# Optimization experiments

Measured on AMD Instinct MI355X. Metric: run time of the kernel, lower is better.

## Reference

```python
import jax, jax.numpy as jnp
import numpy as np

HEADS = 4
EPS_LN = 1e-5
EPS_NORM = 1e-12

def conv1x1(x, w):
    # x: [B,C,T,H,W], w: [O,C] (Conv3d kernel_size=1, no bias)
    return jnp.einsum('oc,bcthw->bothw', w, x)

def dwconv3(x, w):
    # depthwise Conv3d 3x3x3, padding=1; w: [C,1,3,3,3]
    return jax.lax.conv_general_dilated(
        x, w, window_strides=(1, 1, 1), padding='SAME',
        dimension_numbers=('NCDHW', 'OIDHW', 'NCDHW'),
        feature_group_count=x.shape[1])

def layernorm_c(x, w, b):
    # LayerNorm over channel dim (torch LN applied after b c t h w -> b (thw) c)
    m = jnp.mean(x, axis=1, keepdims=True)
    v = jnp.mean(jnp.square(x - m), axis=1, keepdims=True)
    xn = (x - m) * jax.lax.rsqrt(v + EPS_LN)
    return xn * w[None, :, None, None, None] + b[None, :, None, None, None]

def l2norm(x):
    n = jnp.sqrt(jnp.sum(jnp.square(x), axis=-1, keepdims=True))
    return x / jnp.maximum(n, EPS_NORM)

def attention_c(x, qkv_w, qkv_dw_w, proj_w, temperature):
    B, C, T, H, W = x.shape
    qkv = dwconv3(conv1x1(x, qkv_w), qkv_dw_w)  # [B,3C,T,H,W]
    q, k, v = jnp.split(qkv, 3, axis=1)
    def to_heads(a):
        return a.reshape(B, HEADS, C // HEADS, T * H * W)  # b head c (thw)
    q, k, v = to_heads(q), to_heads(k), to_heads(v)
    q = l2norm(q)
    k = l2norm(k)
    # channel attention: [b,h,c,c] score matrix scaled by learnable temperature
    attn = jnp.einsum('bhcn,bhdn->bhcd', q, k) * temperature[None]
    attn = jax.nn.softmax(attn, axis=-1)
    out = jnp.einsum('bhcd,bhdn->bhcn', attn, v)
    out = out.reshape(B, C, T, H, W)
    return conv1x1(out, proj_w)

def feedforward(x, pin_w, ffn_dw_w, pout_w):
    h = conv1x1(x, pin_w)            # [B,2H,T,H,W]
    h = dwconv3(h, ffn_dw_w)
    x1, x2 = jnp.split(h, 2, axis=1)
    g = jax.nn.gelu(x1, approximate=False) * x2
    return conv1x1(g, pout_w)

def setup_inputs() -> dict:
    key = jax.random.key(0)
    ks = jax.random.split(key, 8)
    C, T, H, W = 192, 10, 64, 64
    Hf = int(C * 2.66)  # 510
    s = 0.05
    return {
        'x': jax.random.normal(ks[0], (1, C, T, H, W), jnp.float32),
        'ln1_w': jnp.ones((C,), jnp.float32),
        'ln1_b': jnp.zeros((C,), jnp.float32),
        'qkv_w': jax.random.normal(ks[1], (3 * C, C), jnp.float32) * s,
        'qkv_dw_w': jax.random.normal(ks[2], (3 * C, 1, 3, 3, 3), jnp.float32) * s,
        'proj_w': jax.random.normal(ks[3], (C, C), jnp.float32) * s,
        'temperature': jnp.ones((HEADS, 1, 1), jnp.float32),
        'ln2_w': jnp.ones((C,), jnp.float32),
        'ln2_b': jnp.zeros((C,), jnp.float32),
        'pin_w': jax.random.normal(ks[4], (2 * Hf, C), jnp.float32) * s,
        'ffn_dw_w': jax.random.normal(ks[5], (2 * Hf, 1, 3, 3, 3), jnp.float32) * s,
        'pout_w': jax.random.normal(ks[6], (C, Hf), jnp.float32) * s,
    }

def reference(x, ln1_w, ln1_b, qkv_w, qkv_dw_w, proj_w, temperature,
              ln2_w, ln2_b, pin_w, ffn_dw_w, pout_w):
    y = x + attention_c(layernorm_c(x, ln1_w, ln1_b), qkv_w, qkv_dw_w, proj_w, temperature)
    out = y + feedforward(layernorm_c(y, ln2_w, ln2_b), pin_w, ffn_dw_w, pout_w)
    return out
```

## Files before the change

kernel.cpp:

```cpp
#include <hip/hip_runtime.h>
#include <math.h>

#define NPOS 40960
#define TT 10
#define HH 64
#define WW 64
#define HWP 4096
#define CIN 192
#define C3 576
#define NHEADS 4
#define CHD 48
#define HF 510
#define GNB 80
#define GCHUNK 512

typedef unsigned short u16;
typedef unsigned int   u32;
typedef __bf16 bf16x8 __attribute__((ext_vector_type(8)));
typedef __bf16 bf16x2 __attribute__((ext_vector_type(2)));
typedef float  f32x4  __attribute__((ext_vector_type(4)));
typedef u16    u16x8  __attribute__((ext_vector_type(8)));
typedef u32    u32x4  __attribute__((ext_vector_type(4)));

__device__ __forceinline__ float b2f(u16 u) {
    return __uint_as_float(((unsigned int)u) << 16);
}
__device__ __forceinline__ u16 f2b(float f) {
    unsigned int i = __float_as_uint(f);
    unsigned int r = (i + 0x7FFFu + ((i >> 16) & 1u)) >> 16;
    return (u16)r;
}
__device__ __forceinline__ float gelu_exact(float v) {
    return 0.5f * v * (1.0f + erff(v * 0.70710678118654752f));
}

__device__ __forceinline__ float dot2bf(u32 a, u32 b, float c) {
#if __has_builtin(__builtin_amdgcn_fdot2_f32_bf16)
    return __builtin_amdgcn_fdot2_f32_bf16(
        __builtin_bit_cast(bf16x2, a), __builtin_bit_cast(bf16x2, b), c, false);
#else
    float a0 = b2f((u16)(a & 0xffffu)), a1 = b2f((u16)(a >> 16));
    float b0 = b2f((u16)(b & 0xffffu)), b1 = b2f((u16)(b >> 16));
    return fmaf(a1, b1, fmaf(a0, b0, c));
#endif
}
__device__ __forceinline__ u32 alignp(u32 hi, u32 lo) {
#if __has_builtin(__builtin_amdgcn_alignbit)
    return __builtin_amdgcn_alignbit(hi, lo, 16);
#else
    return (lo >> 16) | (hi << 16);
#endif
}

#define GLD_LDS16(g, l) __builtin_amdgcn_global_load_lds( \
    (const __attribute__((address_space(1))) void*)(g), \
    (__attribute__((address_space(3))) void*)(l), 16, 0, 0)

__global__ void cvt_pad_k(const float* __restrict__ src, u16* __restrict__ dst,
                          int rs, int cs, int rd, int cd) {
    int idx = blockIdx.x * 256 + threadIdx.x;
    if (idx >= rd * cd) return;
    int r = idx / cd, c = idx % cd;
    float v = (r < rs && c < cs) ? src[r * cs + c] : 0.f;
    dst[idx] = f2b(v);
}

template<typename InT>
__global__ __launch_bounds__(256) void lnt_k(const InT* __restrict__ X,
                                             const float* __restrict__ w,
                                             const float* __restrict__ b,
                                             u16* __restrict__ Xt) {
    __shared__ float sm[CIN][65];
    __shared__ float ps[4][64], ps2[4][64];
    __shared__ float smean[64], srstd[64];
    __shared__ float sw[CIN], sb[CIN];
    const int tid = threadIdx.x;
    const int n0 = blockIdx.x * 64;
    if (tid < CIN) { sw[tid] = w[tid]; sb[tid] = b[tid]; }
    if constexpr (sizeof(InT) == 4) {
        #pragma unroll
        for (int i = 0; i < 12; ++i) {
            int e = i * 256 + tid;
            int c = e >> 4, p4 = (e & 15) * 4;
            float4 v = *(const float4*)((const float*)X + (size_t)c * NPOS + n0 + p4);
            sm[c][p4 + 0] = v.x; sm[c][p4 + 1] = v.y;
            sm[c][p4 + 2] = v.z; sm[c][p4 + 3] = v.w;
        }
    } else {
        #pragma unroll
        for (int i = 0; i < 6; ++i) {
            int e = i * 256 + tid;
            int c = e >> 3, p8 = (e & 7) * 8;
            u16x8 v = *(const u16x8*)((const u16*)X + (size_t)c * NPOS + n0 + p8);
            #pragma unroll
            for (int j = 0; j < 8; ++j) sm[c][p8 + j] = b2f(v[j]);
        }
    }
    __syncthreads();
    int g = tid >> 6, nn = tid & 63;
    float s = 0.f, s2 = 0.f;
    for (int c = g * 48; c < g * 48 + 48; ++c) {
        float v = sm[c][nn];
        s += v; s2 += v * v;
    }
    ps[g][nn] = s; ps2[g][nn] = s2;
    __syncthreads();
    if (g == 0) {
        float t = ps[0][nn] + ps[1][nn] + ps[2][nn] + ps[3][nn];
        float t2 = ps2[0][nn] + ps2[1][nn] + ps2[2][nn] + ps2[3][nn];
        float m = t / CIN;
        float var = t2 / CIN - m * m;
        smean[nn] = m;
        srstd[nn] = rsqrtf(var + 1e-5f);
    }
    __syncthreads();
    #pragma unroll
    for (int i = 0; i < 6; ++i) {
        int e = i * 256 + tid;
        int nl = e / 24, cg = e % 24;
        int c0 = cg * 8;
        float m = smean[nl], rs_ = srstd[nl];
        u16x8 o;
        #pragma unroll
        for (int j = 0; j < 8; ++j) {
            float v = (sm[c0 + j][nl] - m) * rs_ * sw[c0 + j] + sb[c0 + j];
            o[j] = f2b(v);
        }
        *(u16x8*)(Xt + (size_t)(n0 + nl) * CIN + c0) = o;
    }
}

__global__ __launch_bounds__(256) void transpose_k(const u16* __restrict__ src,
                                                   u16* __restrict__ dst, int C) {
    __shared__ float sm[64][65];
    const int tid = threadIdx.x;
    const int n0 = blockIdx.x * 64;
    const int cb = blockIdx.y * 64;
    #pragma unroll
    for (int i = 0; i < 2; ++i) {
        int e = i * 256 + tid;
        int cl = e >> 3, nn8 = (e & 7) * 8;
        u16x8 v = *(const u16x8*)(src + (size_t)(cb + cl) * NPOS + n0 + nn8);
        #pragma unroll
        for (int j = 0; j < 8; ++j) sm[cl][nn8 + j] = b2f(v[j]);
    }
    __syncthreads();
    #pragma unroll
    for (int i = 0; i < 2; ++i) {
        int e = i * 256 + tid;
        int nl = e >> 3, c0 = (e & 7) * 8;
        u16x8 o;
        #pragma unroll
        for (int j = 0; j < 8; ++j) o[j] = f2b(sm[c0 + j][nl]);
        *(u16x8*)(dst + (size_t)(n0 + nl) * C + cb + c0) = o;
    }
}

__global__ __launch_bounds__(256) void glu_t_k(const u16* __restrict__ hconv,
                                               u16* __restrict__ gt) {
    __shared__ float sm[64][65];
    const int tid = threadIdx.x;
    const int n0 = blockIdx.x * 64;
    const int cb = blockIdx.y * 64;
    #pragma unroll
    for (int i = 0; i < 2; ++i) {
        int e = i * 256 + tid;
        int cl = e >> 3, nn8 = (e & 7) * 8;
        int c = cb + cl;
        if (c < HF) {
            u16x8 va = *(const u16x8*)(hconv + (size_t)c * NPOS + n0 + nn8);
            u16x8 vb = *(const u16x8*)(hconv + (size_t)(c + HF) * NPOS + n0 + nn8);
            #pragma unroll
            for (int j = 0; j < 8; ++j)
                sm[cl][nn8 + j] = gelu_exact(b2f(va[j])) * b2f(vb[j]);
        } else {
            #pragma unroll
            for (int j = 0; j < 8; ++j) sm[cl][nn8 + j] = 0.f;
        }
    }
    __syncthreads();
    #pragma unroll
    for (int i = 0; i < 2; ++i) {
        int e = i * 256 + tid;
        int nl = e >> 3, c0 = (e & 7) * 8;
        u16x8 o;
        #pragma unroll
        for (int j = 0; j < 8; ++j) o[j] = f2b(sm[c0 + j][nl]);
        *(u16x8*)(gt + (size_t)(n0 + nl) * 512 + cb + c0) = o;
    }
}

template<int KP, typename OutT, typename ResT, bool RESID>
__global__ __launch_bounds__(256) void gemm_mfma_k(
    const u16* __restrict__ A, const u16* __restrict__ Bt, int O,
    const ResT* __restrict__ resid, OutT* __restrict__ outp)
{
    constexpr int NT = KP / 32;
    __shared__ u16 As[2][128 * 32];
    __shared__ u16 Bs[2][128 * 32];
    const int tid  = threadIdx.x;
    const int lane = tid & 63;
    const int wv   = tid >> 6;
    const int lo = lane & 15, hi = lane >> 4;
    const int m_blk = blockIdx.y * 128;
    const int n_blk = blockIdx.x * 128;

    int bb0 = (0 * 4 + wv) * 1024 + lane * 16;
    int bb1 = (1 * 4 + wv) * 1024 + lane * 16;
    const int r0 = bb0 >> 6, c80 = (bb0 >> 4) & 3;
    const int r1 = bb1 >> 6, c81 = (bb1 >> 4) & 3;

    auto stage = [&](int buf, int k0) {
        GLD_LDS16(A  + (size_t)(m_blk + r0) * KP + k0 + c80 * 8, (char*)&As[buf][0] + (0 * 4 + wv) * 1024);
        GLD_LDS16(A  + (size_t)(m_blk + r1) * KP + k0 + c81 * 8, (char*)&As[buf][0] + (1 * 4 + wv) * 1024);
        GLD_LDS16(Bt + (size_t)(n_blk + r0) * KP + k0 + c80 * 8, (char*)&Bs[buf][0] + (0 * 4 + wv) * 1024);
        GLD_LDS16(Bt + (size_t)(n_blk + r1) * KP + k0 + c81 * 8, (char*)&Bs[buf][0] + (1 * 4 + wv) * 1024);
    };

    f32x4 acc[4][4];
    const f32x4 zero = {0.f, 0.f, 0.f, 0.f};
    #pragma unroll
    for (int mt = 0; mt < 4; ++mt)
        #pragma unroll
        for (int nt = 0; nt < 4; ++nt) acc[mt][nt] = zero;

    stage(0, 0);
    __syncthreads();

    #pragma unroll
    for (int t = 0; t < NT; ++t) {
        if (t + 1 < NT) stage((t + 1) & 1, (t + 1) * 32);
        const u16* Ab = &As[t & 1][0] + (wv & 1) * 64 * 32;
        const u16* Bb = &Bs[t & 1][0] + (wv >> 1) * 64 * 32;
        bf16x8 a[4], b[4];
        #pragma unroll
        for (int q = 0; q < 4; ++q) {
            a[q] = *(const bf16x8*)(Ab + (q * 16 + lo) * 32 + hi * 8);
            b[q] = *(const bf16x8*)(Bb + (q * 16 + lo) * 32 + hi * 8);
        }
        #pragma unroll
        for (int mt = 0; mt < 4; ++mt)
            #pragma unroll
            for (int nt = 0; nt < 4; ++nt)
                acc[mt][nt] = __builtin_amdgcn_mfma_f32_16x16x32_bf16(
                    a[mt], b[nt], acc[mt][nt], 0, 0, 0);
        __syncthreads();
    }

    const int m_base = m_blk + (wv & 1) * 64;
    const int n_base = n_blk + (wv >> 1) * 64;
    #pragma unroll
    for (int mt = 0; mt < 4; ++mt) {
        #pragma unroll
        for (int r = 0; r < 4; ++r) {
            int m = m_base + mt * 16 + hi * 4 + r;
            if (m < O) {
                size_t rowoff = (size_t)m * NPOS;
                #pragma unroll
                for (int nt = 0; nt < 4; ++nt) {
                    int n = n_base + nt * 16 + lo;
                    float v = acc[mt][nt][r];
                    if (RESID) {
                        if constexpr (sizeof(ResT) == 2) v += b2f(((const u16*)resid)[rowoff + n]);
                        else                             v += ((const float*)resid)[rowoff + n];
                    }
                    if constexpr (sizeof(OutT) == 2) outp[rowoff + n] = (OutT)f2b(v);
                    else                             outp[rowoff + n] = (OutT)v;
                }
            }
        }
    }
}

__global__ __launch_bounds__(256) void dwconv_k(const u16* __restrict__ in,
                                                u16* __restrict__ outp,
                                                const float* __restrict__ wgt)
{
    const int lane = threadIdx.x & 63;
    const int wv   = threadIdx.x >> 6;
    const int c    = blockIdx.x >> 1;
    const int hb   = blockIdx.x & 1;
    const int h    = hb * 32 + wv * 8 + (lane >> 3);
    const int w0c  = (lane & 7) * 8;
    const bool wl0 = (lane & 7) == 0;
    const bool wl7 = (lane & 7) == 7;
    const bool hup = (h > 0), hdn = (h < HH - 1);
    u32 W01[9], W2h[9];
    {
        const float* wc = wgt + c * 27;
        #pragma unroll
        for (int i = 0; i < 9; ++i) {
            float a = wc[i * 3 + 0], b = wc[i * 3 + 1], d = wc[i * 3 + 2];
            W01[i] = (u32)f2b(a) | ((u32)f2b(b) << 16);
            W2h[i] = ((u32)f2b(d)) << 16;
        }
    }
    const u16* base = in   + (size_t)c * (TT * HWP);
    u16*       ob   = outp + (size_t)c * (TT * HWP);

    u32x4 zv = {0u, 0u, 0u, 0u};
    u32x4 ld[2][3];
    auto issue = [&](int ph, int ts) {
        const u16* rp = base + (size_t)ts * HWP + h * WW + w0c;
        ld[ph][0] = hup ? *(const u32x4*)(rp - WW) : zv;
        ld[ph][1] = *(const u32x4*)(rp);
        ld[ph][2] = hdn ? *(const u32x4*)(rp + WW) : zv;
    };

    float acc[3][8];
    #pragma unroll
    for (int o_ = 0; o_ < 3; ++o_)
        #pragma unroll
        for (int j = 0; j < 8; ++j) acc[o_][j] = 0.f;

    issue(0, 0);
    #pragma unroll
    for (int ts = 0; ts < TT; ++ts) {
        const int cb = ts & 1, nb = cb ^ 1;
        if (ts + 1 < TT) issue(nb, ts + 1);
        #pragma unroll
        for (int dh = 0; dh < 3; ++dh) {
            u32 P0 = ld[cb][dh][0], P1 = ld[cb][dh][1];
            u32 P2 = ld[cb][dh][2], P3 = ld[cb][dh][3];
            u32 Pm = __shfl(P3, lane - 1); Pm = wl0 ? 0u : Pm;
            u32 Pp = __shfl(P0, lane + 1); Pp = wl7 ? 0u : Pp;
            u32 S0 = alignp(P0, Pm), S1 = alignp(P1, P0);
            u32 S2 = alignp(P2, P1), S3 = alignp(P3, P2);
            u32 S4 = alignp(Pp, P3);
            #pragma unroll
            for (int tp = 0; tp < 3; ++tp) {
                int o_;
                if (tp == 2) { if (ts < 1) continue; o_ = (ts - 1) % 3; }
                else if (tp == 1) { o_ = ts % 3; }
                else { if (ts + 1 >= TT) continue; o_ = (ts + 1) % 3; }
                const u32 wA = W01[tp * 3 + dh], wB = W2h[tp * 3 + dh];
                float* ap = acc[o_];
                ap[0] = dot2bf(S0, wA, ap[0]); ap[0] = dot2bf(P0, wB, ap[0]);
                ap[1] = dot2bf(P0, wA, ap[1]); ap[1] = dot2bf(S1, wB, ap[1]);
                ap[2] = dot2bf(S1, wA, ap[2]); ap[2] = dot2bf(P1, wB, ap[2]);
                ap[3] = dot2bf(P1, wA, ap[3]); ap[3] = dot2bf(S2, wB, ap[3]);
                ap[4] = dot2bf(S2, wA, ap[4]); ap[4] = dot2bf(P2, wB, ap[4]);
                ap[5] = dot2bf(P2, wA, ap[5]); ap[5] = dot2bf(S3, wB, ap[5]);
                ap[6] = dot2bf(S3, wA, ap[6]); ap[6] = dot2bf(P3, wB, ap[6]);
                ap[7] = dot2bf(P3, wA, ap[7]); ap[7] = dot2bf(S4, wB, ap[7]);
            }
        }
        if (ts >= 1) {
            u16x8 o;
            #pragma unroll
            for (int j = 0; j < 8; ++j) o[j] = f2b(acc[(ts - 1) % 3][j]);
            *(u16x8*)(ob + (size_t)(ts - 1) * HWP + h * WW + w0c) = o;
            #pragma unroll
            for (int j = 0; j < 8; ++j) acc[(ts - 1) % 3][j] = 0.f;
        }
    }
    u16x8 o;
    #pragma unroll
    for (int j = 0; j < 8; ++j) o[j] = f2b(acc[(TT - 1) % 3][j]);
    *(u16x8*)(ob + (size_t)(TT - 1) * HWP + h * WW + w0c) = o;
}

__global__ void rownorm2_k(const u16* __restrict__ qk, float* __restrict__ norm2) {
    int row = blockIdx.x;
    const u16* p = qk + (size_t)row * NPOS;
    float s = 0.f;
    for (int n = threadIdx.x * 8; n < NPOS; n += 256 * 8) {
        u16x8 v = *(const u16x8*)(p + n);
        #pragma unroll
        for (int j = 0; j < 8; ++j) { float f = b2f(v[j]); s += f * f; }
    }
    __shared__ float red[256];
    red[threadIdx.x] = s; __syncthreads();
    for (int off = 128; off > 0; off >>= 1) {
        if (threadIdx.x < off) red[threadIdx.x] += red[threadIdx.x + off];
        __syncthreads();
    }
    if (threadIdx.x == 0) norm2[row] = red[0];
}

__global__ __launch_bounds__(64) void gram_k(const u16* __restrict__ qkv,
                                             float* __restrict__ part) {
    const int h  = blockIdx.x / GNB;
    const int nb = blockIdx.x % GNB;
    const int lane = threadIdx.x;
    const int lo = lane & 15, hi = lane >> 4;
    const u16* qp = qkv + (size_t)(h * CHD) * NPOS + (size_t)nb * GCHUNK + hi * 8;
    const u16* kp = qkv + (size_t)(CIN + h * CHD) * NPOS + (size_t)nb * GCHUNK + hi * 8;
    f32x4 acc[3][3];
    const f32x4 zero = {0.f, 0.f, 0.f, 0.f};
    #pragma unroll
    for (int mt = 0; mt < 3; ++mt)
        #pragma unroll
        for (int nt = 0; nt < 3; ++nt) acc[mt][nt] = zero;
    #pragma unroll
    for (int ks = 0; ks < GCHUNK; ks += 32) {
        bf16x8 a[3], b[3];
        #pragma unroll
        for (int t = 0; t < 3; ++t) {
            a[t] = *(const bf16x8*)(qp + (size_t)(t * 16 + lo) * NPOS + ks);
            b[t] = *(const bf16x8*)(kp + (size_t)(t * 16 + lo) * NPOS + ks);
        }
        #pragma unroll
        for (int mt = 0; mt < 3; ++mt)
            #pragma unroll
            for (int nt = 0; nt < 3; ++nt)
                acc[mt][nt] = __builtin_amdgcn_mfma_f32_16x16x32_bf16(
                    a[mt], b[nt], acc[mt][nt], 0, 0, 0);
    }
    float* pp = part + (size_t)blockIdx.x * 2304;
    #pragma unroll
    for (int mt = 0; mt < 3; ++mt)
        #pragma unroll
        for (int nt = 0; nt < 3; ++nt)
            #pragma unroll
            for (int r = 0; r < 4; ++r)
                pp[(mt * 16 + hi * 4 + r) * 48 + nt * 16 + lo] = acc[mt][nt][r];
}

__global__ void gram_reduce_k(const float* __restrict__ part, float* __restrict__ S) {
    int idx = blockIdx.x * blockDim.x + threadIdx.x;
    if (idx >= NHEADS * 2304) return;
    int h = idx / 2304, cd = idx % 2304;
    float s = 0.f;
    for (int nb = 0; nb < GNB; ++nb) s += part[(size_t)(h * GNB + nb) * 2304 + cd];
    S[idx] = s;
}

__global__ void softmax_k(const float* __restrict__ S, const float* __restrict__ norm2,
                          const float* __restrict__ temp, float* __restrict__ attn) {
    int row = threadIdx.x;
    if (row >= 192) return;
    int h = row / CHD;
    float qn = fmaxf(sqrtf(norm2[row]), 1e-12f);
    float t = temp[h];
    float vals[48];
    float mx = -1e30f;
    for (int d = 0; d < CHD; ++d) {
        float kn = fmaxf(sqrtf(norm2[CIN + h * CHD + d]), 1e-12f);
        float v = t * S[row * CHD + d] / (qn * kn);
        vals[d] = v; mx = fmaxf(mx, v);
    }
    float sum = 0.f;
    for (int d = 0; d < CHD; ++d) { float e = expf(vals[d] - mx); vals[d] = e; sum += e; }
    float inv = 1.f / sum;
    for (int d = 0; d < CHD; ++d) attn[row * CHD + d] = vals[d] * inv;
}

__global__ void mmat_k(const float* __restrict__ proj_w, const float* __restrict__ attn,
                       float* __restrict__ M) {
    int idx = blockIdx.x * blockDim.x + threadIdx.x;
    if (idx >= CIN * CIN) return;
    int o = idx / CIN, j = idx % CIN;
    int h = j / CHD, d = j % CHD;
    float s = 0.f;
    for (int c = 0; c < CHD; ++c)
        s += proj_w[o * CIN + h * CHD + c] * attn[(h * CHD + c) * CHD + d];
    M[idx] = s;
}

extern "C" void kernel_launch(void* const* d_in, const int* in_sizes, int n_in,
                              void* d_out, int out_size, void* d_ws, size_t ws_size,
                              hipStream_t stream) {
    const float* x       = (const float*)d_in[0];
    const float* ln1w    = (const float*)d_in[1];
    const float* ln1b    = (const float*)d_in[2];
    const float* qkv_w   = (const float*)d_in[3];
    const float* qkv_dw  = (const float*)d_in[4];
    const float* proj_w  = (const float*)d_in[5];
    const float* temp    = (const float*)d_in[6];
    const float* ln2w    = (const float*)d_in[7];
    const float* ln2b    = (const float*)d_in[8];
    const float* pin_w   = (const float*)d_in[9];
    const float* ffn_dw  = (const float*)d_in[10];
    const float* pout_w  = (const float*)d_in[11];
    float* out = (float*)d_out;

    char* wsb = (char*)d_ws;
    size_t off = 0;
    auto alloc = [&](size_t bytes) {
        void* p = wsb + off; off += (bytes + 255) & ~(size_t)255; return p;
    };
    float* norm2   = (float*)alloc(384 * 4);
    float* Sbuf    = (float*)alloc(NHEADS * 2304 * 4);
    float* attn    = (float*)alloc(NHEADS * 2304 * 4);
    float* Mbuf    = (float*)alloc(CIN * CIN * 4);
    float* part    = (float*)alloc((size_t)NHEADS * GNB * 2304 * 4);
    u16*   qkv_wb  = (u16*)alloc((size_t)640 * 192 * 2);
    u16*   pin_wb  = (u16*)alloc((size_t)1024 * 192 * 2);
    u16*   pout_wb = (u16*)alloc((size_t)256 * 512 * 2);
    u16*   M_b     = (u16*)alloc((size_t)256 * 192 * 2);
    u16*   xn1_t   = (u16*)alloc((size_t)NPOS * 192 * 2);
    u16*   yn2_t   = (u16*)alloc((size_t)NPOS * 192 * 2);
    u16*   ybuf    = (u16*)alloc((size_t)CIN * NPOS * 2);
    u16*   regionA = (u16*)alloc((size_t)1024 * NPOS * 2);
    u16*   regionB = (u16*)alloc((size_t)1024 * NPOS * 2);
    u16* qkv_raw  = regionA;
    u16* qkv_conv = regionB;
    u16* h_raw    = regionA;
    u16* h_conv   = regionB;
    u16* gt       = regionA;
    u16* vt       = xn1_t;

    cvt_pad_k<<<(640 * 192 + 255) / 256, 256, 0, stream>>>(qkv_w, qkv_wb, 576, 192, 640, 192);
    cvt_pad_k<<<(1024 * 192 + 255) / 256, 256, 0, stream>>>(pin_w, pin_wb, 1020, 192, 1024, 192);
    cvt_pad_k<<<(256 * 512 + 255) / 256, 256, 0, stream>>>(pout_w, pout_wb, 192, 510, 256, 512);
    lnt_k<float><<<NPOS / 64, 256, 0, stream>>>(x, ln1w, ln1b, xn1_t);
    gemm_mfma_k<192, u16, float, false><<<dim3(NPOS / 128, 5), 256, 0, stream>>>(
        qkv_wb, xn1_t, C3, nullptr, qkv_raw);
    dwconv_k<<<C3 * 2, 256, 0, stream>>>(qkv_raw, qkv_conv, qkv_dw);
    rownorm2_k<<<384, 256, 0, stream>>>(qkv_conv, norm2);
    gram_k<<<NHEADS * GNB, 64, 0, stream>>>(qkv_conv, part);
    gram_reduce_k<<<(NHEADS * 2304 + 255) / 256, 256, 0, stream>>>(part, Sbuf);
    softmax_k<<<1, 192, 0, stream>>>(Sbuf, norm2, temp, attn);
    mmat_k<<<(CIN * CIN + 255) / 256, 256, 0, stream>>>(proj_w, attn, Mbuf);
    cvt_pad_k<<<(256 * 192 + 255) / 256, 256, 0, stream>>>(Mbuf, M_b, 192, 192, 256, 192);
    transpose_k<<<dim3(NPOS / 64, 3), 256, 0, stream>>>(qkv_conv + (size_t)384 * NPOS, vt, 192);
    gemm_mfma_k<192, u16, float, true><<<dim3(NPOS / 128, 2), 256, 0, stream>>>(
        M_b, vt, CIN, x, ybuf);
    lnt_k<u16><<<NPOS / 64, 256, 0, stream>>>(ybuf, ln2w, ln2b, yn2_t);
    gemm_mfma_k<192, u16, float, false><<<dim3(NPOS / 128, 8), 256, 0, stream>>>(
        pin_wb, yn2_t, 1024, nullptr, h_raw);
    dwconv_k<<<1020 * 2, 256, 0, stream>>>(h_raw, h_conv, ffn_dw);
    glu_t_k<<<dim3(NPOS / 64, 8), 256, 0, stream>>>(h_conv, gt);
    gemm_mfma_k<512, float, u16, true><<<dim3(NPOS / 128, 2), 256, 0, stream>>>(
        pout_wb, gt, CIN, ybuf, out);
}
```

Baseline: 262.6 us.

## Fuse GELU gating into FFN dwconv, fold norms into QKV dwconv, merge weight conversions

The FFN depthwise conv now processes both GLU halves per block and writes gelu(x1)*x2 directly. This removes the full 1020-channel conv output write and re-read that the separate GLU/transpose kernel needed. The QKV dwconv accumulates per-row squared norms as it goes, replacing a separate rownorm pass. It also merges the three weight-conversion launches into one, has mmat write padded bf16 directly, and switches to hardware bf16 conversion. In exchange the dwconv_glu kernel holds twice the accumulators and loads, so register pressure rises, and the norm is taken from fp32 values rather than bf16-rounded ones.

Result: faster. 252.5 us (-3.8%).

```diff
diff --git a/kernel.cpp b/kernel.cpp
--- a/kernel.cpp
+++ b/kernel.cpp
@@ -30,6 +30,9 @@
     unsigned int r = (i + 0x7FFFu + ((i >> 16) & 1u)) >> 16;
     return (u16)r;
 }
+__device__ __forceinline__ u16 f2bh(float f) {
+    return __builtin_bit_cast(u16, static_cast<__bf16>(f));
+}
 __device__ __forceinline__ float gelu_exact(float v) {
     return 0.5f * v * (1.0f + erff(v * 0.70710678118654752f));
 }
@@ -56,13 +59,26 @@
     (const __attribute__((address_space(1))) void*)(g), \
     (__attribute__((address_space(3))) void*)(l), 16, 0, 0)
 
-__global__ void cvt_pad_k(const float* __restrict__ src, u16* __restrict__ dst,
-                          int rs, int cs, int rd, int cd) {
+#define CVT_N1 (640 * 192)
+#define CVT_N2 (1024 * 192)
+#define CVT_N3 (256 * 512)
+__global__ void cvtw_k(const float* __restrict__ qkv_w, const float* __restrict__ pin_w,
+                       const float* __restrict__ pout_w,
+                       u16* __restrict__ qkv_wb, u16* __restrict__ pin_wb,
+                       u16* __restrict__ pout_wb) {
     int idx = blockIdx.x * 256 + threadIdx.x;
-    if (idx >= rd * cd) return;
-    int r = idx / cd, c = idx % cd;
-    float v = (r < rs && c < cs) ? src[r * cs + c] : 0.f;
-    dst[idx] = f2b(v);
+    if (idx < CVT_N1) {
+        int r = idx / 192, c = idx % 192;
+        qkv_wb[idx] = f2bh(r < 576 ? qkv_w[r * 192 + c] : 0.f);
+    } else if (idx < CVT_N1 + CVT_N2) {
+        int k = idx - CVT_N1;
+        int r = k / 192, c = k % 192;
+        pin_wb[k] = f2bh(r < 1020 ? pin_w[r * 192 + c] : 0.f);
+    } else if (idx < CVT_N1 + CVT_N2 + CVT_N3) {
+        int k = idx - CVT_N1 - CVT_N2;
+        int r = k / 512, c = k % 512;
+        pout_wb[k] = f2bh((r < 192 && c < 510) ? pout_w[r * 510 + c] : 0.f);
+    }
 }
 
 template<typename InT>
@@ -124,14 +140,15 @@
         #pragma unroll
         for (int j = 0; j < 8; ++j) {
             float v = (sm[c0 + j][nl] - m) * rs_ * sw[c0 + j] + sb[c0 + j];
-            o[j] = f2b(v);
+            o[j] = f2bh(v);
         }
         *(u16x8*)(Xt + (size_t)(n0 + nl) * CIN + c0) = o;
     }
 }
 
-__global__ __launch_bounds__(256) void transpose_k(const u16* __restrict__ src,
-                                                   u16* __restrict__ dst, int C) {
+__global__ __launch_bounds__(256) void transpose_pad_k(const u16* __restrict__ src,
+                                                       u16* __restrict__ dst,
+                                                       int CS, int CD) {
     __shared__ float sm[64][65];
     const int tid = threadIdx.x;
     const int n0 = blockIdx.x * 64;
@@ -140,9 +157,15 @@
     for (int i = 0; i < 2; ++i) {
         int e = i * 256 + tid;
         int cl = e >> 3, nn8 = (e & 7) * 8;
-        u16x8 v = *(const u16x8*)(src + (size_t)(cb + cl) * NPOS + n0 + nn8);
-        #pragma unroll
-        for (int j = 0; j < 8; ++j) sm[cl][nn8 + j] = b2f(v[j]);
+        int c = cb + cl;
+        if (c < CS) {
+            u16x8 v = *(const u16x8*)(src + (size_t)c * NPOS + n0 + nn8);
+            #pragma unroll
+            for (int j = 0; j < 8; ++j) sm[cl][nn8 + j] = b2f(v[j]);
+        } else {
+            #pragma unroll
+            for (int j = 0; j < 8; ++j) sm[cl][nn8 + j] = 0.f;
+        }
     }
     __syncthreads();
     #pragma unroll
@@ -151,42 +174,8 @@
         int nl = e >> 3, c0 = (e & 7) * 8;
         u16x8 o;
         #pragma unroll
-        for (int j = 0; j < 8; ++j) o[j] = f2b(sm[c0 + j][nl]);
-        *(u16x8*)(dst + (size_t)(n0 + nl) * C + cb + c0) = o;
-    }
-}
-
-__global__ __launch_bounds__(256) void glu_t_k(const u16* __restrict__ hconv,
-                                               u16* __restrict__ gt) {
-    __shared__ float sm[64][65];
-    const int tid = threadIdx.x;
-    const int n0 = blockIdx.x * 64;
-    const int cb = blockIdx.y * 64;
-    #pragma unroll
-    for (int i = 0; i < 2; ++i) {
-        int e = i * 256 + tid;
-        int cl = e >> 3, nn8 = (e & 7) * 8;
-        int c = cb + cl;
-        if (c < HF) {
-            u16x8 va = *(const u16x8*)(hconv + (size_t)c * NPOS + n0 + nn8);
-            u16x8 vb = *(const u16x8*)(hconv + (size_t)(c + HF) * NPOS + n0 + nn8);
-            #pragma unroll
-            for (int j = 0; j < 8; ++j)
-                sm[cl][nn8 + j] = gelu_exact(b2f(va[j])) * b2f(vb[j]);
-        } else {
-            #pragma unroll
-            for (int j = 0; j < 8; ++j) sm[cl][nn8 + j] = 0.f;
-        }
-    }
-    __syncthreads();
-    #pragma unroll
-    for (int i = 0; i < 2; ++i) {
-        int e = i * 256 + tid;
-        int nl = e >> 3, c0 = (e & 7) * 8;
-        u16x8 o;
-        #pragma unroll
-        for (int j = 0; j < 8; ++j) o[j] = f2b(sm[c0 + j][nl]);
-        *(u16x8*)(gt + (size_t)(n0 + nl) * 512 + cb + c0) = o;
+        for (int j = 0; j < 8; ++j) o[j] = f2bh(sm[c0 + j][nl]);
+        *(u16x8*)(dst + (size_t)(n0 + nl) * CD + cb + c0) = o;
     }
 }
 
@@ -264,7 +253,7 @@
                         if constexpr (sizeof(ResT) == 2) v += b2f(((const u16*)resid)[rowoff + n]);
                         else                             v += ((const float*)resid)[rowoff + n];
                     }
-                    if constexpr (sizeof(OutT) == 2) outp[rowoff + n] = (OutT)f2b(v);
+                    if constexpr (sizeof(OutT) == 2) outp[rowoff + n] = (OutT)f2bh(v);
                     else                             outp[rowoff + n] = (OutT)v;
                 }
             }
@@ -274,8 +263,10 @@
 
 __global__ __launch_bounds__(256) void dwconv_k(const u16* __restrict__ in,
                                                 u16* __restrict__ outp,
-                                                const float* __restrict__ wgt)
+                                                const float* __restrict__ wgt,
+                                                float* __restrict__ nrm2)
 {
+    __shared__ float red[256];
     const int lane = threadIdx.x & 63;
     const int wv   = threadIdx.x >> 6;
     const int c    = blockIdx.x >> 1;
@@ -312,6 +303,7 @@
     for (int o_ = 0; o_ < 3; ++o_)
         #pragma unroll
         for (int j = 0; j < 8; ++j) acc[o_][j] = 0.f;
+    float sq = 0.f;
 
     issue(0, 0);
     #pragma unroll
@@ -346,36 +338,145 @@
             }
         }
         if (ts >= 1) {
+            const int o_ = (ts - 1) % 3;
             u16x8 o;
             #pragma unroll
-            for (int j = 0; j < 8; ++j) o[j] = f2b(acc[(ts - 1) % 3][j]);
+            for (int j = 0; j < 8; ++j) {
+                float v = acc[o_][j];
+                sq = fmaf(v, v, sq);
+                o[j] = f2bh(v);
+            }
             *(u16x8*)(ob + (size_t)(ts - 1) * HWP + h * WW + w0c) = o;
             #pragma unroll
-            for (int j = 0; j < 8; ++j) acc[(ts - 1) % 3][j] = 0.f;
-        }
-    }
-    u16x8 o;
-    #pragma unroll
-    for (int j = 0; j < 8; ++j) o[j] = f2b(acc[(TT - 1) % 3][j]);
-    *(u16x8*)(ob + (size_t)(TT - 1) * HWP + h * WW + w0c) = o;
-}
-
-__global__ void rownorm2_k(const u16* __restrict__ qk, float* __restrict__ norm2) {
-    int row = blockIdx.x;
-    const u16* p = qk + (size_t)row * NPOS;
-    float s = 0.f;
-    for (int n = threadIdx.x * 8; n < NPOS; n += 256 * 8) {
-        u16x8 v = *(const u16x8*)(p + n);
-        #pragma unroll
-        for (int j = 0; j < 8; ++j) { float f = b2f(v[j]); s += f * f; }
-    }
-    __shared__ float red[256];
-    red[threadIdx.x] = s; __syncthreads();
-    for (int off = 128; off > 0; off >>= 1) {
-        if (threadIdx.x < off) red[threadIdx.x] += red[threadIdx.x + off];
+            for (int j = 0; j < 8; ++j) acc[o_][j] = 0.f;
+        }
+    }
+    {
+        const int o_ = (TT - 1) % 3;
+        u16x8 o;
+        #pragma unroll
+        for (int j = 0; j < 8; ++j) {
+            float v = acc[o_][j];
+            sq = fmaf(v, v, sq);
+            o[j] = f2bh(v);
+        }
+        *(u16x8*)(ob + (size_t)(TT - 1) * HWP + h * WW + w0c) = o;
+    }
+    if (nrm2) {
+        red[threadIdx.x] = sq;
         __syncthreads();
-    }
-    if (threadIdx.x == 0) norm2[row] = red[0];
+        for (int off = 128; off > 0; off >>= 1) {
+            if (threadIdx.x < off) red[threadIdx.x] += red[threadIdx.x + off];
+            __syncthreads();
+        }
+        if (threadIdx.x == 0) nrm2[c * 2 + hb] = red[0];
+    }
+}
+
+__global__ __launch_bounds__(256) void dwconv_glu_k(const u16* __restrict__ in,
+                                                    u16* __restrict__ gout,
+                                                    const float* __restrict__ wgt)
+{
+    const int lane = threadIdx.x & 63;
+    const int wv   = threadIdx.x >> 6;
+    const int c    = blockIdx.x >> 1;
+    const int hb   = blockIdx.x & 1;
+    const int h    = hb * 32 + wv * 8 + (lane >> 3);
+    const int w0c  = (lane & 7) * 8;
+    const bool wl0 = (lane & 7) == 0;
+    const bool wl7 = (lane & 7) == 7;
+    const bool hup = (h > 0), hdn = (h < HH - 1);
+
+    u32 W01[2][9], W2h[2][9];
+    #pragma unroll
+    for (int ch = 0; ch < 2; ++ch) {
+        const float* wc = wgt + (size_t)(c + ch * HF) * 27;
+        #pragma unroll
+        for (int i = 0; i < 9; ++i) {
+            float a = wc[i * 3 + 0], b = wc[i * 3 + 1], d = wc[i * 3 + 2];
+            W01[ch][i] = (u32)f2b(a) | ((u32)f2b(b) << 16);
+            W2h[ch][i] = ((u32)f2b(d)) << 16;
+        }
+    }
+    const u16* base0 = in + (size_t)c * (TT * HWP);
+    const u16* base1 = in + (size_t)(c + HF) * (TT * HWP);
+    u16* ob = gout + (size_t)c * (TT * HWP);
+
+    u32x4 zv = {0u, 0u, 0u, 0u};
+    u32x4 ld[2][2][3];
+    auto issue = [&](int ph, int ts) {
+        const u16* rp0 = base0 + (size_t)ts * HWP + h * WW + w0c;
+        ld[0][ph][0] = hup ? *(const u32x4*)(rp0 - WW) : zv;
+        ld[0][ph][1] = *(const u32x4*)(rp0);
+        ld[0][ph][2] = hdn ? *(const u32x4*)(rp0 + WW) : zv;
+        const u16* rp1 = base1 + (size_t)ts * HWP + h * WW + w0c;
+        ld[1][ph][0] = hup ? *(const u32x4*)(rp1 - WW) : zv;
+        ld[1][ph][1] = *(const u32x4*)(rp1);
+        ld[1][ph][2] = hdn ? *(const u32x4*)(rp1 + WW) : zv;
+    };
+
+    float acc[2][3][8];
+    #pragma unroll
+    for (int ch = 0; ch < 2; ++ch)
+        #pragma unroll
+        for (int o_ = 0; o_ < 3; ++o_)
+            #pragma unroll
+            for (int j = 0; j < 8; ++j) acc[ch][o_][j] = 0.f;
+
+    issue(0, 0);
+    #pragma unroll
+    for (int ts = 0; ts < TT; ++ts) {
+        const int cb = ts & 1, nb = cb ^ 1;
+        if (ts + 1 < TT) issue(nb, ts + 1);
+        #pragma unroll
+        for (int ch = 0; ch < 2; ++ch) {
+            #pragma unroll
+            for (int dh = 0; dh < 3; ++dh) {
+                u32 P0 = ld[ch][cb][dh][0], P1 = ld[ch][cb][dh][1];
+                u32 P2 = ld[ch][cb][dh][2], P3 = ld[ch][cb][dh][3];
+                u32 Pm = __shfl(P3, lane - 1); Pm = wl0 ? 0u : Pm;
+                u32 Pp = __shfl(P0, lane + 1); Pp = wl7 ? 0u : Pp;
+                u32 S0 = alignp(P0, Pm), S1 = alignp(P1, P0);
+                u32 S2 = alignp(P2, P1), S3 = alignp(P3, P2);
+                u32 S4 = alignp(Pp, P3);
+                #pragma unroll
+                for (int tp = 0; tp < 3; ++tp) {
+                    int o_;
+                    if (tp == 2) { if (ts < 1) continue; o_ = (ts - 1) % 3; }
+                    else if (tp == 1) { o_ = ts % 3; }
+                    else { if (ts + 1 >= TT) continue; o_ = (ts + 1) % 3; }
+                    const u32 wA = W01[ch][tp * 3 + dh], wB = W2h[ch][tp * 3 + dh];
+                    float* ap = acc[ch][o_];
+                    ap[0] = dot2bf(S0, wA, ap[0]); ap[0] = dot2bf(P0, wB, ap[0]);
+                    ap[1] = dot2bf(P0, wA, ap[1]); ap[1] = dot2bf(S1, wB, ap[1]);
+                    ap[2] = dot2bf(S1, wA, ap[2]); ap[2] = dot2bf(P1, wB, ap[2]);
+                    ap[3] = dot2bf(P1, wA, ap[3]); ap[3] = dot2bf(S2, wB, ap[3]);
+                    ap[4] = dot2bf(S2, wA, ap[4]); ap[4] = dot2bf(P2, wB, ap[4]);
+                    ap[5] = dot2bf(P2, wA, ap[5]); ap[5] = dot2bf(S3, wB, ap[5]);
+                    ap[6] = dot2bf(S3, wA, ap[6]); ap[6] = dot2bf(P3, wB, ap[6]);
+                    ap[7] = dot2bf(P3, wA, ap[7]); ap[7] = dot2bf(S4, wB, ap[7]);
+                }
+            }
+        }
+        if (ts >= 1) {
+            const int o_ = (ts - 1) % 3;
+            u16x8 o;
+            #pragma unroll
+            for (int j = 0; j < 8; ++j)
+                o[j] = f2bh(gelu_exact(acc[0][o_][j]) * acc[1][o_][j]);
+            *(u16x8*)(ob + (size_t)(ts - 1) * HWP + h * WW + w0c) = o;
+            #pragma unroll
+            for (int j = 0; j < 8; ++j) { acc[0][o_][j] = 0.f; acc[1][o_][j] = 0.f; }
+        }
+    }
+    {
+        const int o_ = (TT - 1) % 3;
+        u16x8 o;
+        #pragma unroll
+        for (int j = 0; j < 8; ++j)
+            o[j] = f2bh(gelu_exact(acc[0][o_][j]) * acc[1][o_][j]);
+        *(u16x8*)(ob + (size_t)(TT - 1) * HWP + h * WW + w0c) = o;
+    }
 }
 
 __global__ __launch_bounds__(64) void gram_k(const u16* __restrict__ qkv,
@@ -426,17 +527,18 @@
     S[idx] = s;
 }
 
-__global__ void softmax_k(const float* __restrict__ S, const float* __restrict__ norm2,
+__global__ void softmax_k(const float* __restrict__ S, const float* __restrict__ norm2p,
                           const float* __restrict__ temp, float* __restrict__ attn) {
     int row = threadIdx.x;
     if (row >= 192) return;
     int h = row / CHD;
-    float qn = fmaxf(sqrtf(norm2[row]), 1e-12f);
+    float qn = fmaxf(sqrtf(norm2p[2 * row] + norm2p[2 * row + 1]), 1e-12f);
     float t = temp[h];
     float vals[48];
     float mx = -1e30f;
     for (int d = 0; d < CHD; ++d) {
-        float kn = fmaxf(sqrtf(norm2[CIN + h * CHD + d]), 1e-12f);
+        int kc = CIN + h * CHD + d;
+        float kn = fmaxf(sqrtf(norm2p[2 * kc] + norm2p[2 * kc + 1]), 1e-12f);
         float v = t * S[row * CHD + d] / (qn * kn);
         vals[d] = v; mx = fmaxf(mx, v);
     }
@@ -447,15 +549,17 @@
 }
 
 __global__ void mmat_k(const float* __restrict__ proj_w, const float* __restrict__ attn,
-                       float* __restrict__ M) {
+                       u16* __restrict__ Mb) {
     int idx = blockIdx.x * blockDim.x + threadIdx.x;
-    if (idx >= CIN * CIN) return;
+    if (idx >= 256 * CIN) return;
     int o = idx / CIN, j = idx % CIN;
-    int h = j / CHD, d = j % CHD;
     float s = 0.f;
-    for (int c = 0; c < CHD; ++c)
-        s += proj_w[o * CIN + h * CHD + c] * attn[(h * CHD + c) * CHD + d];
-    M[idx] = s;
+    if (o < CIN) {
+        int h = j / CHD, d = j % CHD;
+        for (int c = 0; c < CHD; ++c)
+            s += proj_w[o * CIN + h * CHD + c] * attn[(h * CHD + c) * CHD + d];
+    }
+    Mb[idx] = f2bh(s);
 }
 
 extern "C" void kernel_launch(void* const* d_in, const int* in_sizes, int n_in,
@@ -480,10 +584,9 @@
     auto alloc = [&](size_t bytes) {
         void* p = wsb + off; off += (bytes + 255) & ~(size_t)255; return p;
     };
-    float* norm2   = (float*)alloc(384 * 4);
+    float* norm2p  = (float*)alloc(C3 * 2 * 4);
     float* Sbuf    = (float*)alloc(NHEADS * 2304 * 4);
     float* attn    = (float*)alloc(NHEADS * 2304 * 4);
-    float* Mbuf    = (float*)alloc(CIN * CIN * 4);
     float* part    = (float*)alloc((size_t)NHEADS * GNB * 2304 * 4);
     u16*   qkv_wb  = (u16*)alloc((size_t)640 * 192 * 2);
     u16*   pin_wb  = (u16*)alloc((size_t)1024 * 192 * 2);
@@ -497,31 +600,29 @@
     u16* qkv_raw  = regionA;
     u16* qkv_conv = regionB;
     u16* h_raw    = regionA;
-    u16* h_conv   = regionB;
+    u16* g510     = regionB;
     u16* gt       = regionA;
     u16* vt       = xn1_t;
 
-    cvt_pad_k<<<(640 * 192 + 255) / 256, 256, 0, stream>>>(qkv_w, qkv_wb, 576, 192, 640, 192);
-    cvt_pad_k<<<(1024 * 192 + 255) / 256, 256, 0, stream>>>(pin_w, pin_wb, 1020, 192, 1024, 192);
-    cvt_pad_k<<<(256 * 512 + 255) / 256, 256, 0, stream>>>(pout_w, pout_wb, 192, 510, 256, 512);
+    cvtw_k<<<(CVT_N1 + CVT_N2 + CVT_N3 + 255) / 256, 256, 0, stream>>>(
+        qkv_w, pin_w, pout_w, qkv_wb, pin_wb, pout_wb);
     lnt_k<float><<<NPOS / 64, 256, 0, stream>>>(x, ln1w, ln1b, xn1_t);
     gemm_mfma_k<192, u16, float, false><<<dim3(NPOS / 128, 5), 256, 0, stream>>>(
         qkv_wb, xn1_t, C3, nullptr, qkv_raw);
-    dwconv_k<<<C3 * 2, 256, 0, stream>>>(qkv_raw, qkv_conv, qkv_dw);
-    rownorm2_k<<<384, 256, 0, stream>>>(qkv_conv, norm2);
+    dwconv_k<<<C3 * 2, 256, 0, stream>>>(qkv_raw, qkv_conv, qkv_dw, norm2p);
     gram_k<<<NHEADS * GNB, 64, 0, stream>>>(qkv_conv, part);
     gram_reduce_k<<<(NHEADS * 2304 + 255) / 256, 256, 0, stream>>>(part, Sbuf);
-    softmax_k<<<1, 192, 0, stream>>>(Sbuf, norm2, temp, attn);
-    mmat_k<<<(CIN * CIN + 255) / 256, 256, 0, stream>>>(proj_w, attn, Mbuf);
-    cvt_pad_k<<<(256 * 192 + 255) / 256, 256, 0, stream>>>(Mbuf, M_b, 192, 192, 256, 192);
-    transpose_k<<<dim3(NPOS / 64, 3), 256, 0, stream>>>(qkv_conv + (size_t)384 * NPOS, vt, 192);
+    softmax_k<<<1, 192, 0, stream>>>(Sbuf, norm2p, temp, attn);
+    mmat_k<<<(256 * CIN + 255) / 256, 256, 0, stream>>>(proj_w, attn, M_b);
+    transpose_pad_k<<<dim3(NPOS / 64, 3), 256, 0, stream>>>(
+        qkv_conv + (size_t)384 * NPOS, vt, 192, 192);
     gemm_mfma_k<192, u16, float, true><<<dim3(NPOS / 128, 2), 256, 0, stream>>>(
         M_b, vt, CIN, x, ybuf);
     lnt_k<u16><<<NPOS / 64, 256, 0, stream>>>(ybuf, ln2w, ln2b, yn2_t);
     gemm_mfma_k<192, u16, float, false><<<dim3(NPOS / 128, 8), 256, 0, stream>>>(
         pin_wb, yn2_t, 1024, nullptr, h_raw);
-    dwconv_k<<<1020 * 2, 256, 0, stream>>>(h_raw, h_conv, ffn_dw);
-    glu_t_k<<<dim3(NPOS / 64, 8), 256, 0, stream>>>(h_conv, gt);
+    dwconv_glu_k<<<HF * 2, 256, 0, stream>>>(h_raw, g510, ffn_dw);
+    transpose_pad_k<<<dim3(NPOS / 64, 8), 256, 0, stream>>>(g510, gt, HF, 512);
     gemm_mfma_k<512, float, u16, true><<<dim3(NPOS / 128, 2), 256, 0, stream>>>(
         pout_wb, gt, CIN, ybuf, out);
 }
```
